# Optimization experiments

Hardware: AMD Instinct MI355X
Metric: run time of the kernel (lower is better)

The kernel has to match this reference:

```python
import jax, jax.numpy as jnp
import numpy as np

N_NODES = 20000
E_RAND = 300000
IN_F, OUT_F, HEADS = 1280, 128, 4
HID = OUT_F * HEADS  # 512


def gat_conv(x, src, dst, W, attn_l, attn_r, bias, n_nodes):
    """DGL GATConv: fc (no bias) -> per-edge LeakyReLU(el_src+er_dst) ->
    segment softmax over incoming edges -> weighted scatter-sum -> +bias.
    Returns (N, HEADS, OUT_F)."""
    h = (x @ W).reshape(n_nodes, HEADS, OUT_F)            # (N,H,F)
    el = jnp.einsum('nhf,hf->nh', h, attn_l)              # (N,H)
    er = jnp.einsum('nhf,hf->nh', h, attn_r)              # (N,H)
    e = jax.nn.leaky_relu(el[src] + er[dst], 0.2)         # (E,H)
    emax = jax.ops.segment_max(e, dst, num_segments=n_nodes)
    ee = jnp.exp(e - emax[dst])                           # (E,H)
    denom = jax.ops.segment_sum(ee, dst, num_segments=n_nodes)
    alpha = ee / denom[dst]                               # (E,H)
    msg = h[src] * alpha[:, :, None]                      # (E,H,F)
    out = jax.ops.segment_sum(msg, dst, num_segments=n_nodes)
    return out + bias.reshape(HEADS, OUT_F)


def setup_inputs() -> dict:
    key = jax.random.key(0)
    ks = jax.random.split(key, 12)
    src_r = jax.random.randint(ks[0], (E_RAND,), 0, N_NODES)
    dst_r = jax.random.randint(ks[1], (E_RAND,), 0, N_NODES)
    self_loop = jnp.arange(N_NODES)
    src = jnp.concatenate([src_r, self_loop])  # self loops: contact[i][i]=1
    dst = jnp.concatenate([dst_r, self_loop])
    feature = jax.random.normal(ks[2], (N_NODES, IN_F), dtype=jnp.float32)
    s1 = 1.0 / np.sqrt(IN_F)
    s2 = 1.0 / np.sqrt(HID)
    return {
        'feature': feature,
        'W1': jax.random.normal(ks[3], (IN_F, HID), dtype=jnp.float32) * s1,
        'al1': jax.random.normal(ks[4], (HEADS, OUT_F), dtype=jnp.float32) * s2,
        'ar1': jax.random.normal(ks[5], (HEADS, OUT_F), dtype=jnp.float32) * s2,
        'b1': jnp.zeros((HID,), dtype=jnp.float32),
        'W2': jax.random.normal(ks[6], (HID, HID), dtype=jnp.float32) * s2,
        'al2': jax.random.normal(ks[7], (HEADS, OUT_F), dtype=jnp.float32) * s2,
        'ar2': jax.random.normal(ks[8], (HEADS, OUT_F), dtype=jnp.float32) * s2,
        'b2': jnp.zeros((HID,), dtype=jnp.float32),
        'Wfc': jax.random.normal(ks[9], (HID, 64), dtype=jnp.float32) * s2,
        'bfc': jnp.zeros((64,), dtype=jnp.float32),
        'src': src,
        'dst': dst,
    }


def reference(feature, W1, al1, ar1, b1, W2, al2, ar2, b2, Wfc, bfc, src, dst):
    n = feature.shape[0]
    out = gat_conv(feature, src, dst, W1, al1, ar1, b1, n)   # (N,4,128)
    out = jax.nn.elu(out).reshape(n, HID)                    # (N,512)
    out = gat_conv(out, src, dst, W2, al2, ar2, b2, n)       # (N,4,128)
    out = jax.nn.elu(out).reshape(n, HID)                    # (N,512)
    out = out @ Wfc + bfc                                    # (N,64)
    out = jax.nn.elu(out[None, :, :])                        # (1,N,64)
    return out
```

## Files before the change

kernel.cpp:

```cpp
#include <hip/hip_runtime.h>
#include <hip/hip_bf16.h>
#include <math.h>

#define HID 512
#define HEADS 4
#define OUTF 128

typedef __attribute__((ext_vector_type(8))) _Float16 f16x8_t;
typedef __attribute__((ext_vector_type(4))) _Float16 f16x4_t;
typedef __attribute__((ext_vector_type(4))) float f32x4_t;

__device__ __forceinline__ void gl_lds16(const void* g, void* l) {
    __builtin_amdgcn_global_load_lds(
        (const __attribute__((address_space(1))) void*)g,
        (__attribute__((address_space(3))) void*)l, 16, 0, 0);
}

__device__ __forceinline__ void stage_plane64(const _Float16* g, int strideE,
    int rbase, int rmax, char* plane, int tid)
{
#pragma unroll
    for (int j = 0; j < 4; ++j) {
        int gci = j * 256 + tid;
        int r = gci >> 3, c = gci & 7;
        int rg = rbase + r; if (rg > rmax) rg = rmax;
        const char* s = (const char*)(g + (size_t)rg * strideE) + ((c ^ (r & 7)) << 4);
        char* d = plane + (j * 256 + (tid & ~63)) * 16;
        gl_lds16(s, d);
    }
}

__global__ __launch_bounds__(256) void conv_hist_kernel(const float* __restrict__ in,
    _Float16* __restrict__ o, int nquad,
    const int* __restrict__ dst, int* __restrict__ deg, int E)
{
    const int stride = gridDim.x * 256;
    const int t0 = blockIdx.x * 256 + threadIdx.x;
    for (int i = t0; i < nquad; i += stride) {
        float4 v = *(const float4*)&in[(size_t)i * 4];
        f16x4_t ov;
        ov[0] = (_Float16)v.x; ov[1] = (_Float16)v.y;
        ov[2] = (_Float16)v.z; ov[3] = (_Float16)v.w;
        *(f16x4_t*)&o[(size_t)i * 4] = ov;
    }
    for (int e = t0; e < E; e += stride) atomicAdd(&deg[dst[e]], 1);
}

__global__ __launch_bounds__(256) void fill_prep_kernel(
    const int* __restrict__ srcv, const int* __restrict__ dstv,
    const int* __restrict__ offs, int* __restrict__ cursor,
    int* __restrict__ psrc, int E, int fillB,
    const float* __restrict__ W1, _Float16* __restrict__ W1t,
    const float* __restrict__ W2, _Float16* __restrict__ W2t,
    const float* __restrict__ Wfc, _Float16* __restrict__ Wft)
{
    __shared__ float tile[32][33];
    const int b = blockIdx.x;
    if (b < fillB) {
        int e = b * 256 + threadIdx.x;
        if (e < E) {
            int d = dstv[e];
            int p = atomicAdd(&cursor[d], 1);
            psrc[offs[d] + p] = srcv[e];
        }
        return;
    }
    int pb = b - fillB;
    const float* W; _Float16* Wt; int K, NC, bx, by;
    if (pb < 640)      { W = W1;  Wt = W1t; K = 1280; NC = 512; bx = pb % 40; by = pb / 40; }
    else if (pb < 896) { pb -= 640; W = W2;  Wt = W2t; K = 512; NC = 512; bx = pb & 15; by = pb >> 4; }
    else               { pb -= 896; W = Wfc; Wt = Wft; K = 512; NC = 64;  bx = pb & 15; by = pb >> 4; }
    const int k0 = bx * 32, n0 = by * 32;
    const int t = threadIdx.x;
    {
        int r = t >> 3, c4 = (t & 7) * 4;
        float4 v = *(const float4*)&W[(size_t)(k0 + r) * NC + n0 + c4];
        tile[r][c4] = v.x; tile[r][c4 + 1] = v.y;
        tile[r][c4 + 2] = v.z; tile[r][c4 + 3] = v.w;
    }
    __syncthreads();
    int n = t >> 3, kc = (t & 7) * 4;
#pragma unroll
    for (int i = 0; i < 4; ++i)
        Wt[(size_t)(n0 + n) * K + k0 + kc + i] = (_Float16)tile[kc + i][n];
}

template<int EPI, int OUT16, int ELER>
__global__ __launch_bounds__(256, 4) void gemm_f16(
    const _Float16* __restrict__ Af, const _Float16* __restrict__ Bt,
    const float* __restrict__ bias,
    const float* __restrict__ attl, const float* __restrict__ attr,
    float* __restrict__ elp, float* __restrict__ erp,
    void* __restrict__ Cout, int M, int K, int NCOL, int ldC,
    int ncolT, int nwg)
{
    __shared__ char lds[32768];
    char* const APL = lds;
    char* const BPL = lds + 16384;
    const int tid = threadIdx.x;
    const int wave = tid >> 6, lane = tid & 63;
    const int wm = wave >> 1, wn = wave & 1;
    const int b = blockIdx.x;
    const int q = nwg >> 3, rr = nwg & 7;
    const int xcd = b & 7, ib = b >> 3;
    const int logical = (xcd < rr ? xcd * (q + 1) : rr * (q + 1) + (xcd - rr) * q) + ib;
    const int bm = (logical / ncolT) * 128, bcol = logical % ncolT;
    const int bn = bcol * 128;
    const int l15 = lane & 15, l4 = lane >> 4;
    const int swz7 = l15 & 7;

    f32x4_t acc[4][4];
#pragma unroll
    for (int i = 0; i < 4; ++i)
#pragma unroll
        for (int j = 0; j < 4; ++j) acc[i][j] = (f32x4_t){0.f, 0.f, 0.f, 0.f};

    const int nt = K >> 6;
    for (int t = 0; t < nt; ++t) {
        stage_plane64(Af + t * 64, K, bm, M - 1, APL, tid);
        stage_plane64(Bt + t * 64, K, bn, NCOL - 1, BPL, tid);
        __syncthreads();
#pragma unroll
        for (int ks = 0; ks < 2; ++ks) {
            f16x8_t fa[4], fb[4];
#pragma unroll
            for (int mf = 0; mf < 4; ++mf) {
                int row = wm * 64 + mf * 16 + l15;
                fa[mf] = *(const f16x8_t*)(APL + row * 128 + (((ks * 4 + l4) ^ swz7) << 4));
            }
#pragma unroll
            for (int nf = 0; nf < 4; ++nf) {
                int rn = wn * 64 + nf * 16 + l15;
                fb[nf] = *(const f16x8_t*)(BPL + rn * 128 + (((ks * 4 + l4) ^ swz7) << 4));
            }
#pragma unroll
            for (int mf = 0; mf < 4; ++mf)
#pragma unroll
                for (int nf = 0; nf < 4; ++nf)
                    acc[mf][nf] = __builtin_amdgcn_mfma_f32_16x16x32_f16(fa[mf], fb[nf], acc[mf][nf], 0, 0, 0);
        }
        __syncthreads();
    }

#pragma unroll
    for (int mf = 0; mf < 4; ++mf) {
        int rbase = bm + wm * 64 + mf * 16 + l4 * 4;
#pragma unroll
        for (int nf = 0; nf < 4; ++nf) {
            int col = bn + wn * 64 + nf * 16 + l15;
            if (col >= NCOL) continue;
#pragma unroll
            for (int r = 0; r < 4; ++r) {
                int row = rbase + r;
                if (row < M) {
                    float v = acc[mf][nf][r];
                    if (EPI) {
                        v += bias[col];
                        v = v > 0.f ? v : (expf(v) - 1.f);
                    }
                    if (OUT16) ((_Float16*)Cout)[(size_t)row * ldC + col] = (_Float16)v;
                    else       ((float*)Cout)[(size_t)row * ldC + col] = v;
                }
            }
        }
    }
    if (ELER) {
        const int head = bcol;
        float alv[4], arv[4];
#pragma unroll
        for (int nf = 0; nf < 4; ++nf) {
            int cl = wn * 64 + nf * 16 + l15;
            alv[nf] = attl[head * OUTF + cl];
            arv[nf] = attr[head * OUTF + cl];
        }
        float pel[4][4], perr[4][4];
#pragma unroll
        for (int mf = 0; mf < 4; ++mf)
#pragma unroll
            for (int r = 0; r < 4; ++r) {
                float se = 0.f, sr = 0.f;
#pragma unroll
                for (int nf = 0; nf < 4; ++nf) {
                    se = fmaf(acc[mf][nf][r], alv[nf], se);
                    sr = fmaf(acc[mf][nf][r], arv[nf], sr);
                }
                pel[mf][r] = se; perr[mf][r] = sr;
            }
#pragma unroll
        for (int off = 1; off < 16; off <<= 1)
#pragma unroll
            for (int mf = 0; mf < 4; ++mf)
#pragma unroll
                for (int r = 0; r < 4; ++r) {
                    pel[mf][r]  += __shfl_xor(pel[mf][r],  off);
                    perr[mf][r] += __shfl_xor(perr[mf][r], off);
                }
        __syncthreads();
        float* red = (float*)lds;
        if (l15 == 0) {
#pragma unroll
            for (int mf = 0; mf < 4; ++mf)
#pragma unroll
                for (int r = 0; r < 4; ++r) {
                    int rl = wm * 64 + mf * 16 + l4 * 4 + r;
                    red[rl * 2 + wn]       = pel[mf][r];
                    red[256 + rl * 2 + wn] = perr[mf][r];
                }
        }
        __syncthreads();
        if (tid < 128) {
            int row = bm + tid;
            if (row < M) {
                float es = red[tid * 2] + red[tid * 2 + 1];
                float rs = red[256 + tid * 2] + red[256 + tid * 2 + 1];
                elp[row * HEADS + head] = es;
                erp[row * HEADS + head] = rs;
            }
        }
    }
}

__global__ __launch_bounds__(256) void scan1_kernel(const int* __restrict__ deg,
    int* __restrict__ offs, int* __restrict__ bsum, int N)
{
    __shared__ int buf[256];
    int tid = threadIdx.x;
    int i = blockIdx.x * 256 + tid;
    int v = (i < N) ? deg[i] : 0;
    buf[tid] = v;
    __syncthreads();
#pragma unroll
    for (int off = 1; off < 256; off <<= 1) {
        int t = (tid >= off) ? buf[tid - off] : 0;
        __syncthreads();
        buf[tid] += t;
        __syncthreads();
    }
    if (i < N) offs[i] = buf[tid] - v;
    if (tid == 255) bsum[blockIdx.x] = buf[255];
}

__global__ void scan2_kernel(int* __restrict__ bsum, int nb)
{
    if (threadIdx.x == 0) {
        int acc = 0;
        for (int b = 0; b < nb; ++b) { int t = bsum[b]; bsum[b] = acc; acc += t; }
        bsum[nb] = acc;
    }
}

__global__ void scan3_kernel(int* __restrict__ offs, const int* __restrict__ bsum,
                             int N, int nb)
{
    int i = blockIdx.x * 256 + threadIdx.x;
    if (i < N) offs[i] += bsum[blockIdx.x];
    if (i == 0) offs[N] = bsum[nb];
}

__global__ __launch_bounds__(256) void aggregate_kernel(const _Float16* __restrict__ h,
    const int* __restrict__ offs, const int* __restrict__ psrc,
    const float* __restrict__ el, const float* __restrict__ er,
    const float* __restrict__ bias, _Float16* __restrict__ xo, int N)
{
    const int n = blockIdx.x * 4 + (threadIdx.x >> 6);
    if (n >= N) return;
    const int lane = threadIdx.x & 63;
    const int c = lane * 8;
    const int head = lane >> 4;
    const int hp = lane >> 5;
    const int e31 = lane & 31;
    const int sbase = (head >> 1) << 5;
    const int hsel = head & 1;

    const float2 er2 = *(const float2*)&er[n * HEADS + hp * 2];

    float acc[8];
#pragma unroll
    for (int k = 0; k < 8; ++k) acc[k] = 0.f;
    float ws = 0.f;

    const int beg = offs[n], end = offs[n + 1];
    for (int base = beg; base < end; base += 32) {
        const int cnt = min(32, end - base);
        int idx = base + e31;
        if (e31 >= cnt) idx = beg;
        const int s = psrc[idx];
        const float2 lv = *(const float2*)&el[s * HEADS + hp * 2];
        float x0 = lv.x + er2.x; x0 = x0 > 0.f ? x0 : 0.2f * x0;
        float x1 = lv.y + er2.y; x1 = x1 > 0.f ? x1 : 0.2f * x1;
        const float wa = expf(x0);
        const float wb = expf(x1);

        int j = 0;
        for (; j + 4 <= cnt; j += 4) {
            int s0 = __shfl(s, j);     int s1 = __shfl(s, j + 1);
            int s2 = __shfl(s, j + 2); int s3 = __shfl(s, j + 3);
            float a0 = __shfl(wa, sbase + j),     b0 = __shfl(wb, sbase + j);
            float a1 = __shfl(wa, sbase + j + 1), b1 = __shfl(wb, sbase + j + 1);
            float a2 = __shfl(wa, sbase + j + 2), b2 = __shfl(wb, sbase + j + 2);
            float a3 = __shfl(wa, sbase + j + 3), b3 = __shfl(wb, sbase + j + 3);
            float w0 = hsel ? b0 : a0;
            float w1 = hsel ? b1 : a1;
            float w2 = hsel ? b2 : a2;
            float w3 = hsel ? b3 : a3;
            f16x8_t v0 = *(const f16x8_t*)&h[(size_t)s0 * HID + c];
            f16x8_t v1 = *(const f16x8_t*)&h[(size_t)s1 * HID + c];
            f16x8_t v2 = *(const f16x8_t*)&h[(size_t)s2 * HID + c];
            f16x8_t v3 = *(const f16x8_t*)&h[(size_t)s3 * HID + c];
#pragma unroll
            for (int k = 0; k < 8; ++k) {
                acc[k] = fmaf(w0, (float)v0[k], acc[k]);
                acc[k] = fmaf(w1, (float)v1[k], acc[k]);
                acc[k] = fmaf(w2, (float)v2[k], acc[k]);
                acc[k] = fmaf(w3, (float)v3[k], acc[k]);
            }
            ws += w0 + w1 + w2 + w3;
        }
        for (; j < cnt; ++j) {
            int s0 = __shfl(s, j);
            float a0 = __shfl(wa, sbase + j), b0 = __shfl(wb, sbase + j);
            float w0 = hsel ? b0 : a0;
            f16x8_t v0 = *(const f16x8_t*)&h[(size_t)s0 * HID + c];
#pragma unroll
            for (int k = 0; k < 8; ++k) acc[k] = fmaf(w0, (float)v0[k], acc[k]);
            ws += w0;
        }
    }
    float inv = 1.f / ws;
    float4 b0v = *(const float4*)&bias[c];
    float4 b1v = *(const float4*)&bias[c + 4];
    float bb[8] = {b0v.x, b0v.y, b0v.z, b0v.w, b1v.x, b1v.y, b1v.z, b1v.w};
    f16x8_t ov;
#pragma unroll
    for (int k = 0; k < 8; ++k) {
        float r = acc[k] * inv + bb[k];
        r = r > 0.f ? r : (expf(r) - 1.f);
        ov[k] = (_Float16)r;
    }
    *(f16x8_t*)&xo[(size_t)n * HID + c] = ov;
}

extern "C" void kernel_launch(void* const* d_in, const int* in_sizes, int n_in,
                              void* d_out, int out_size, void* d_ws, size_t ws_size,
                              hipStream_t stream)
{
    const float* feature = (const float*)d_in[0];
    const float* W1  = (const float*)d_in[1];
    const float* al1 = (const float*)d_in[2];
    const float* ar1 = (const float*)d_in[3];
    const float* b1  = (const float*)d_in[4];
    const float* W2  = (const float*)d_in[5];
    const float* al2 = (const float*)d_in[6];
    const float* ar2 = (const float*)d_in[7];
    const float* b2  = (const float*)d_in[8];
    const float* Wfc = (const float*)d_in[9];
    const float* bfc = (const float*)d_in[10];
    const int* src = (const int*)d_in[11];
    const int* dst = (const int*)d_in[12];
    const int N = in_sizes[0] / 1280;
    const int E = in_sizes[11];
    const int nb = (N + 255) / 256;
    float* out = (float*)d_out;

    char* ws = (char*)d_ws;
    size_t off = 0;
    auto alloc = [&](size_t bytes) {
        void* p = ws + off;
        off += (bytes + 255) & ~(size_t)255;
        return p;
    };
    const size_t degsz = ((size_t)N * 4 + 255) & ~(size_t)255;
    int* deg    = (int*)alloc((size_t)N * 4);
    int* cursor = (int*)alloc((size_t)N * 4);
    int* offs   = (int*)alloc((size_t)(N + 1) * 4);
    int* bsum   = (int*)alloc((size_t)(nb + 1) * 4);
    float* el   = (float*)alloc((size_t)N * HEADS * 4);
    float* er   = (float*)alloc((size_t)N * HEADS * 4);
    int* psrc   = (int*)alloc((size_t)E * 4);
    _Float16* featf = (_Float16*)alloc((size_t)N * 1280 * 2);
    _Float16* hbuf  = (_Float16*)alloc((size_t)N * HID * 2);
    _Float16* xh    = (_Float16*)alloc((size_t)N * HID * 2);
    _Float16* W1t   = (_Float16*)alloc((size_t)HID * 1280 * 2);
    _Float16* W2t   = (_Float16*)alloc((size_t)HID * HID * 2);
    _Float16* Wft   = (_Float16*)alloc((size_t)64 * HID * 2);

    hipMemsetAsync(deg, 0, degsz * 2, stream);
    conv_hist_kernel<<<2048, 256, 0, stream>>>(feature, featf, N * 1280 / 4,
                                               dst, deg, E);
    scan1_kernel<<<nb, 256, 0, stream>>>(deg, offs, bsum, N);
    scan2_kernel<<<1, 64, 0, stream>>>(bsum, nb);
    scan3_kernel<<<nb, 256, 0, stream>>>(offs, bsum, N, nb);
    const int fillB = (E + 255) / 256;
    fill_prep_kernel<<<fillB + 928, 256, 0, stream>>>(src, dst, offs, cursor,
                                                      psrc, E, fillB,
                                                      W1, W1t, W2, W2t, Wfc, Wft);

    const int nrowT = (N + 127) / 128;
    const int nwgG = nrowT * 4;
    const int nwgF = nrowT;
    const int aggB = (N + 3) / 4;

    gemm_f16<0, 1, 1><<<nwgG, 256, 0, stream>>>(featf, W1t, nullptr,
                                                al1, ar1, el, er,
                                                hbuf, N, 1280, HID, HID,
                                                4, nwgG);
    aggregate_kernel<<<aggB, 256, 0, stream>>>(hbuf, offs, psrc, el, er, b1, xh, N);

    gemm_f16<0, 1, 1><<<nwgG, 256, 0, stream>>>(xh, W2t, nullptr,
                                                al2, ar2, el, er,
                                                hbuf, N, HID, HID, HID,
                                                4, nwgG);
    aggregate_kernel<<<aggB, 256, 0, stream>>>(hbuf, offs, psrc, el, er, b2, xh, N);

    gemm_f16<1, 0, 0><<<nwgF, 256, 0, stream>>>(xh, Wft, bfc,
                                                nullptr, nullptr, nullptr, nullptr,
                                                out, N, HID, 64, 64,
                                                1, nwgF);
}
```

Measured before the change: 243.0 us.

## Use 256x256 double-buffered GEMM tiles for the GAT projection layers

Replaces the 128x128 single-buffered f16 MFMA GEMM used for the two GAT projections with a 512-thread kernel that computes 256x256 tiles and double-buffers K-slices in 128KB of LDS. The next K-slice is prefetched while the current one is consumed. The larger tile raises operand reuse per global load and cuts the number of workgroups, while el/er head reductions are still fused in the epilogue. The trade-offs are heavy LDS and register use per block (lower occupancy) and fewer workgroups (about 158), which may under-fill the 256 CUs. The final FC layer moves to its own specialised kernel.

```diff
diff --git a/kernel.cpp b/kernel.cpp
--- a/kernel.cpp
+++ b/kernel.cpp
@@ -16,16 +16,17 @@
         (__attribute__((address_space(3))) void*)l, 16, 0, 0);
 }
 
-__device__ __forceinline__ void stage_plane64(const _Float16* g, int strideE,
+template<int ROWS, int THREADS>
+__device__ __forceinline__ void stage64(const _Float16* g, int strideE,
     int rbase, int rmax, char* plane, int tid)
 {
 #pragma unroll
-    for (int j = 0; j < 4; ++j) {
-        int gci = j * 256 + tid;
+    for (int j = 0; j < ROWS * 8 / THREADS; ++j) {
+        int gci = j * THREADS + tid;
         int r = gci >> 3, c = gci & 7;
         int rg = rbase + r; if (rg > rmax) rg = rmax;
         const char* s = (const char*)(g + (size_t)rg * strideE) + ((c ^ (r & 7)) << 4);
-        char* d = plane + (j * 256 + (tid & ~63)) * 16;
+        char* d = plane + (j * THREADS + (tid & ~63)) * 16;
         gl_lds16(s, d);
     }
 }
@@ -85,14 +86,141 @@
         Wt[(size_t)(n0 + n) * K + k0 + kc + i] = (_Float16)tile[kc + i][n];
 }
 
-template<int EPI, int OUT16, int ELER>
-__global__ __launch_bounds__(256, 4) void gemm_f16(
+__global__ __launch_bounds__(512, 2) void gemm256(
     const _Float16* __restrict__ Af, const _Float16* __restrict__ Bt,
-    const float* __restrict__ bias,
     const float* __restrict__ attl, const float* __restrict__ attr,
     float* __restrict__ elp, float* __restrict__ erp,
-    void* __restrict__ Cout, int M, int K, int NCOL, int ldC,
-    int ncolT, int nwg)
+    _Float16* __restrict__ Cout, int M, int K, int nwg)
+{
+    __shared__ char lds[131072];
+    const int tid = threadIdx.x;
+    const int wave = tid >> 6, lane = tid & 63;
+    const int wm = wave >> 2, wn = wave & 3;
+    const int b = blockIdx.x;
+    const int q = nwg >> 3, rr = nwg & 7;
+    const int xcd = b & 7, ib = b >> 3;
+    const int logical = (xcd < rr ? xcd * (q + 1) : rr * (q + 1) + (xcd - rr) * q) + ib;
+    const int bm = (logical >> 1) * 256;
+    const int bcol = logical & 1;
+    const int bn = bcol * 256;
+    const int l15 = lane & 15, l4 = lane >> 4;
+
+    f32x4_t acc[8][4];
+#pragma unroll
+    for (int i = 0; i < 8; ++i)
+#pragma unroll
+        for (int j = 0; j < 4; ++j) acc[i][j] = (f32x4_t){0.f, 0.f, 0.f, 0.f};
+
+    const int nt = K >> 6;
+    stage64<256, 512>(Af, K, bm, M - 1, lds, tid);
+    stage64<256, 512>(Bt, K, bn, HID - 1, lds + 32768, tid);
+    __syncthreads();
+
+    for (int t = 0; t < nt; ++t) {
+        char* APL = lds + (t & 1) * 65536;
+        char* BPL = APL + 32768;
+        if (t + 1 < nt) {
+            char* NXT = lds + ((t + 1) & 1) * 65536;
+            stage64<256, 512>(Af + (t + 1) * 64, K, bm, M - 1, NXT, tid);
+            stage64<256, 512>(Bt + (t + 1) * 64, K, bn, HID - 1, NXT + 32768, tid);
+        }
+#pragma unroll
+        for (int ks = 0; ks < 2; ++ks) {
+            f16x8_t fa[8], fb[4];
+#pragma unroll
+            for (int mf = 0; mf < 8; ++mf) {
+                int row = wm * 128 + mf * 16 + l15;
+                fa[mf] = *(const f16x8_t*)(APL + row * 128 + (((ks * 4 + l4) ^ (l15 & 7)) << 4));
+            }
+#pragma unroll
+            for (int nf = 0; nf < 4; ++nf) {
+                int rn = wn * 64 + nf * 16 + l15;
+                fb[nf] = *(const f16x8_t*)(BPL + rn * 128 + (((ks * 4 + l4) ^ (l15 & 7)) << 4));
+            }
+#pragma unroll
+            for (int mf = 0; mf < 8; ++mf)
+#pragma unroll
+                for (int nf = 0; nf < 4; ++nf)
+                    acc[mf][nf] = __builtin_amdgcn_mfma_f32_16x16x32_f16(fa[mf], fb[nf], acc[mf][nf], 0, 0, 0);
+        }
+        __syncthreads();
+    }
+
+#pragma unroll
+    for (int mf = 0; mf < 8; ++mf) {
+        int rbase = bm + wm * 128 + mf * 16 + l4 * 4;
+#pragma unroll
+        for (int nf = 0; nf < 4; ++nf) {
+            int col = bn + wn * 64 + nf * 16 + l15;
+#pragma unroll
+            for (int r = 0; r < 4; ++r) {
+                int row = rbase + r;
+                if (row < M) Cout[(size_t)row * HID + col] = (_Float16)acc[mf][nf][r];
+            }
+        }
+    }
+    {
+        const int head = bcol * 2 + (wn >> 1);
+        float alv[4], arv[4];
+#pragma unroll
+        for (int nf = 0; nf < 4; ++nf) {
+            int cl = (wn & 1) * 64 + nf * 16 + l15;
+            alv[nf] = attl[head * OUTF + cl];
+            arv[nf] = attr[head * OUTF + cl];
+        }
+        float pel[8][4], perr[8][4];
+#pragma unroll
+        for (int mf = 0; mf < 8; ++mf)
+#pragma unroll
+            for (int r = 0; r < 4; ++r) {
+                float se = 0.f, sr = 0.f;
+#pragma unroll
+                for (int nf = 0; nf < 4; ++nf) {
+                    se = fmaf(acc[mf][nf][r], alv[nf], se);
+                    sr = fmaf(acc[mf][nf][r], arv[nf], sr);
+                }
+                pel[mf][r] = se; perr[mf][r] = sr;
+            }
+#pragma unroll
+        for (int off = 1; off < 16; off <<= 1)
+#pragma unroll
+            for (int mf = 0; mf < 8; ++mf)
+#pragma unroll
+                for (int r = 0; r < 4; ++r) {
+                    pel[mf][r]  += __shfl_xor(pel[mf][r],  off);
+                    perr[mf][r] += __shfl_xor(perr[mf][r], off);
+                }
+        __syncthreads();
+        float* red = (float*)lds;
+        if (l15 == 0) {
+#pragma unroll
+            for (int mf = 0; mf < 8; ++mf)
+#pragma unroll
+                for (int r = 0; r < 4; ++r) {
+                    int rl = wm * 128 + mf * 16 + l4 * 4 + r;
+                    red[rl * 4 + wn]        = pel[mf][r];
+                    red[1024 + rl * 4 + wn] = perr[mf][r];
+                }
+        }
+        __syncthreads();
+        {
+            int rl = tid & 255;
+            int hh = tid >> 8;
+            int row = bm + rl;
+            if (row < M) {
+                float es = red[rl * 4 + hh * 2] + red[rl * 4 + hh * 2 + 1];
+                float rs = red[1024 + rl * 4 + hh * 2] + red[1024 + rl * 4 + hh * 2 + 1];
+                elp[row * HEADS + bcol * 2 + hh] = es;
+                erp[row * HEADS + bcol * 2 + hh] = rs;
+            }
+        }
+    }
+}
+
+__global__ __launch_bounds__(256, 4) void gemm_fc(
+    const _Float16* __restrict__ Af, const _Float16* __restrict__ Bt,
+    const float* __restrict__ bias, float* __restrict__ Cout,
+    int M, int K, int NCOL, int nwg)
 {
     __shared__ char lds[32768];
     char* const APL = lds;
@@ -104,10 +232,8 @@
     const int q = nwg >> 3, rr = nwg & 7;
     const int xcd = b & 7, ib = b >> 3;
     const int logical = (xcd < rr ? xcd * (q + 1) : rr * (q + 1) + (xcd - rr) * q) + ib;
-    const int bm = (logical / ncolT) * 128, bcol = logical % ncolT;
-    const int bn = bcol * 128;
+    const int bm = logical * 128;
     const int l15 = lane & 15, l4 = lane >> 4;
-    const int swz7 = l15 & 7;
 
     f32x4_t acc[4][4];
 #pragma unroll
@@ -117,8 +243,8 @@
 
     const int nt = K >> 6;
     for (int t = 0; t < nt; ++t) {
-        stage_plane64(Af + t * 64, K, bm, M - 1, APL, tid);
-        stage_plane64(Bt + t * 64, K, bn, NCOL - 1, BPL, tid);
+        stage64<128, 256>(Af + t * 64, K, bm, M - 1, APL, tid);
+        stage64<128, 256>(Bt + t * 64, K, 0, NCOL - 1, BPL, tid);
         __syncthreads();
 #pragma unroll
         for (int ks = 0; ks < 2; ++ks) {
@@ -126,12 +252,12 @@
 #pragma unroll
             for (int mf = 0; mf < 4; ++mf) {
                 int row = wm * 64 + mf * 16 + l15;
-                fa[mf] = *(const f16x8_t*)(APL + row * 128 + (((ks * 4 + l4) ^ swz7) << 4));
+                fa[mf] = *(const f16x8_t*)(APL + row * 128 + (((ks * 4 + l4) ^ (l15 & 7)) << 4));
             }
 #pragma unroll
             for (int nf = 0; nf < 4; ++nf) {
                 int rn = wn * 64 + nf * 16 + l15;
-                fb[nf] = *(const f16x8_t*)(BPL + rn * 128 + (((ks * 4 + l4) ^ swz7) << 4));
+                fb[nf] = *(const f16x8_t*)(BPL + rn * 128 + (((ks * 4 + l4) ^ (l15 & 7)) << 4));
             }
 #pragma unroll
             for (int mf = 0; mf < 4; ++mf)
@@ -141,80 +267,21 @@
         }
         __syncthreads();
     }
-
 #pragma unroll
     for (int mf = 0; mf < 4; ++mf) {
         int rbase = bm + wm * 64 + mf * 16 + l4 * 4;
 #pragma unroll
         for (int nf = 0; nf < 4; ++nf) {
-            int col = bn + wn * 64 + nf * 16 + l15;
+            int col = wn * 64 + nf * 16 + l15;
             if (col >= NCOL) continue;
 #pragma unroll
             for (int r = 0; r < 4; ++r) {
                 int row = rbase + r;
                 if (row < M) {
-                    float v = acc[mf][nf][r];
-                    if (EPI) {
-                        v += bias[col];
-                        v = v > 0.f ? v : (expf(v) - 1.f);
-                    }
-                    if (OUT16) ((_Float16*)Cout)[(size_t)row * ldC + col] = (_Float16)v;
-                    else       ((float*)Cout)[(size_t)row * ldC + col] = v;
+                    float v = acc[mf][nf][r] + bias[col];
+                    v = v > 0.f ? v : (expf(v) - 1.f);
+                    Cout[(size_t)row * NCOL + col] = v;
                 }
-            }
-        }
-    }
-    if (ELER) {
-        const int head = bcol;
-        float alv[4], arv[4];
-#pragma unroll
-        for (int nf = 0; nf < 4; ++nf) {
-            int cl = wn * 64 + nf * 16 + l15;
-            alv[nf] = attl[head * OUTF + cl];
-            arv[nf] = attr[head * OUTF + cl];
-        }
-        float pel[4][4], perr[4][4];
-#pragma unroll
-        for (int mf = 0; mf < 4; ++mf)
-#pragma unroll
-            for (int r = 0; r < 4; ++r) {
-                float se = 0.f, sr = 0.f;
-#pragma unroll
-                for (int nf = 0; nf < 4; ++nf) {
-                    se = fmaf(acc[mf][nf][r], alv[nf], se);
-                    sr = fmaf(acc[mf][nf][r], arv[nf], sr);
-                }
-                pel[mf][r] = se; perr[mf][r] = sr;
-            }
-#pragma unroll
-        for (int off = 1; off < 16; off <<= 1)
-#pragma unroll
-            for (int mf = 0; mf < 4; ++mf)
-#pragma unroll
-                for (int r = 0; r < 4; ++r) {
-                    pel[mf][r]  += __shfl_xor(pel[mf][r],  off);
-                    perr[mf][r] += __shfl_xor(perr[mf][r], off);
-                }
-        __syncthreads();
-        float* red = (float*)lds;
-        if (l15 == 0) {
-#pragma unroll
-            for (int mf = 0; mf < 4; ++mf)
-#pragma unroll
-                for (int r = 0; r < 4; ++r) {
-                    int rl = wm * 64 + mf * 16 + l4 * 4 + r;
-                    red[rl * 2 + wn]       = pel[mf][r];
-                    red[256 + rl * 2 + wn] = perr[mf][r];
-                }
-        }
-        __syncthreads();
-        if (tid < 128) {
-            int row = bm + tid;
-            if (row < M) {
-                float es = red[tid * 2] + red[tid * 2 + 1];
-                float rs = red[256 + tid * 2] + red[256 + tid * 2 + 1];
-                elp[row * HEADS + head] = es;
-                erp[row * HEADS + head] = rs;
             }
         }
     }
@@ -395,25 +462,18 @@
                                                       psrc, E, fillB,
                                                       W1, W1t, W2, W2t, Wfc, Wft);
 
-    const int nrowT = (N + 127) / 128;
-    const int nwgG = nrowT * 4;
-    const int nwgF = nrowT;
+    const int nrow256 = (N + 255) / 256;
+    const int nwgG = nrow256 * 2;
+    const int nwgF = (N + 127) / 128;
     const int aggB = (N + 3) / 4;
 
-    gemm_f16<0, 1, 1><<<nwgG, 256, 0, stream>>>(featf, W1t, nullptr,
-                                                al1, ar1, el, er,
-                                                hbuf, N, 1280, HID, HID,
-                                                4, nwgG);
+    gemm256<<<nwgG, 512, 0, stream>>>(featf, W1t, al1, ar1, el, er,
+                                      hbuf, N, 1280, nwgG);
     aggregate_kernel<<<aggB, 256, 0, stream>>>(hbuf, offs, psrc, el, er, b1, xh, N);
 
-    gemm_f16<0, 1, 1><<<nwgG, 256, 0, stream>>>(xh, W2t, nullptr,
-                                                al2, ar2, el, er,
-                                                hbuf, N, HID, HID, HID,
-                                                4, nwgG);
+    gemm256<<<nwgG, 512, 0, stream>>>(xh, W2t, al2, ar2, el, er,
+                                      hbuf, N, HID, nwgG);
     aggregate_kernel<<<aggB, 256, 0, stream>>>(hbuf, offs, psrc, el, er, b2, xh, N);
 
-    gemm_f16<1, 0, 0><<<nwgF, 256, 0, stream>>>(xh, Wft, bfc,
-                                                nullptr, nullptr, nullptr, nullptr,
-                                                out, N, HID, 64, 64,
-                                                1, nwgF);
-}
+    gemm_fc<<<nwgF, 256, 0, stream>>>(xh, Wft, bfc, out, N, HID, 64, nwgF);
+}
```

Result: slower. 254.3 us (+4.7%).
